# Kernel optimization log

Measured on AMD Instinct MI355X. Metric: run time of the kernel, lower is better.

## Reference

```python
import jax, jax.numpy as jnp
from jax import lax
import numpy as np

ITER_ = 10
SMOOTH = 1.0

# ---------- soft skeletonization (clDice-style, 2D) ----------

def _max_pool(x, wh, ww):
    # x: [B,1,H,W]
    return lax.reduce_window(x, -jnp.inf, lax.max, (1, 1, wh, ww), (1, 1, 1, 1), 'SAME')

def _soft_erode(x):
    return jnp.minimum(-_max_pool(-x, 3, 1), -_max_pool(-x, 1, 3))

def _soft_dilate(x):
    return _max_pool(x, 3, 3)

def _soft_open(x):
    return _soft_dilate(_soft_erode(x))

def soft_skel(img, iters):
    skel = jax.nn.relu(img - _soft_open(img))
    for _ in range(iters):
        img = _soft_erode(img)
        delta = jax.nn.relu(img - _soft_open(img))
        skel = skel + jax.nn.relu(delta - skel * delta)
    return skel

# ---------- exact 2D Euclidean distance transform ----------

def _edt2d(mask):
    # mask: [H,W] bool, True = foreground. distance to nearest background pixel.
    H, W = mask.shape
    BIG = jnp.float32(H + W)
    z = ~mask  # background indicator
    def step(d, zr):
        d = jnp.where(zr, 0.0, jnp.minimum(d + 1.0, BIG))
        return d, d
    init = jnp.full((H,), BIG, jnp.float32)
    _, f = lax.scan(step, init, z.T)            # [W,H] forward along rows
    _, b = lax.scan(step, init, z.T[::-1])      # backward
    g = jnp.minimum(f, b[::-1]).T               # [H,W] 1D row distance
    ys = jnp.arange(H, dtype=jnp.float32)
    diff2 = (ys[:, None] - ys[None, :]) ** 2    # [H,H]
    # lower envelope over columns: d2[y,x] = min_y' g[y',x]^2 + (y-y')^2
    d2 = jnp.min(g[None, :, :] ** 2 + diff2[:, :, None], axis=1)  # [H,W]
    return jnp.sqrt(d2)

_edt_batched = jax.vmap(_edt2d)  # [B,H,W] bool -> [B,H,W] float

# ---------- cbDice pieces ----------

def combine_tensors(A, B, C):
    return jnp.where((A != 0) & (B == 0), A * C, B * C)

def get_weights(mask_input, skel_input, prob_flag):
    # mask_input/skel_input: [B,H,W] float
    mask = mask_input > 0.5
    skel = skel_input > 0.5
    dist = lax.stop_gradient(_edt_batched(mask))       # EDT of binary mask, non-diff
    distances = jnp.where(mask, dist, 0.0)
    skel_radius = jnp.where(skel, distances, 0.0)
    rmax = jnp.maximum(jnp.max(skel_radius, axis=(1, 2), keepdims=True), 1.0)
    rmin = jnp.maximum(jnp.min(skel_radius, axis=(1, 2), keepdims=True), 1.0)
    d_clip = jnp.minimum(distances, rmax)
    dist_map_norm = d_clip / rmax
    skel_R_norm = skel_radius / rmax
    I_norm = (rmax - skel_radius + rmin) / rmax        # dim == 2 branch
    I_norm = jnp.where(skel, I_norm, 0.0)
    if prob_flag:
        return dist_map_norm * mask_input, skel_R_norm * mask_input, I_norm * skel_input
    m = mask.astype(jnp.float32)
    s = skel.astype(jnp.float32)
    return dist_map_norm * m, skel_R_norm * m, I_norm * s

def soft_cb_dice_loss(y_pred, y_true):
    p = jax.nn.sigmoid(y_pred)                              # [B,1,H,W]
    pb = jnp.concatenate([1.0 - p, p], axis=1)              # [B,2,H,W]
    pp = jax.nn.softmax(pb, axis=1)[:, 1]                   # [B,H,W]
    yt = jnp.where(y_true > 0, 1.0, 0.0)[:, 0]              # [B,H,W]
    hard = lax.stop_gradient((pp > 0.5).astype(jnp.float32))
    skel_pred_hard = lax.stop_gradient(soft_skel(hard[:, None], ITER_)[:, 0])
    skel_true = lax.stop_gradient(soft_skel(yt[:, None], ITER_)[:, 0])
    skel_pred_prob = skel_pred_hard * pp
    q_vl, q_slvl, q_sl = get_weights(yt, skel_true, False)
    q_vp, q_spvp, q_sp = get_weights(pp, skel_pred_prob, True)
    w_tprec = (jnp.sum(q_sp * q_vl) + SMOOTH) / (jnp.sum(combine_tensors(q_spvp, q_slvl, q_sp)) + SMOOTH)
    w_tsens = (jnp.sum(q_sl * q_vp) + SMOOTH) / (jnp.sum(combine_tensors(q_slvl, q_spvp, q_sl)) + SMOOTH)
    return 1.0 - 2.0 * (w_tprec * w_tsens) / (w_tprec + w_tsens)

def setup_inputs() -> dict:
    key = jax.random.key(0)
    k1, k2 = jax.random.split(key)
    y_pred = jax.random.normal(k1, (4, 1, 256, 256), dtype=jnp.float32)
    y_true = jax.random.randint(k2, (4, 1, 256, 256), 0, 2, dtype=jnp.int32)
    return {"y_pred": y_pred, "y_true": y_true}

def reference(y_pred, y_true):
    return soft_cb_dice_loss(y_pred, y_true)
```

## Files before the change

### kernel.cpp

```cpp
#include <hip/hip_runtime.h>

typedef unsigned long long u64;

#define NIMG 4
#define H 256
#define W 256
#define NPIX (H*W)
#define NTOT (NIMG*NPIX)
#define WPR 4
#define WPI (H*WPR)
#define WPB (NIMG*WPI)
#define XT 8
#define NSKEL 8
#define NTILE 128
#define NB2 (NSKEL+NTILE)

#define CFLAG(bi)  ((bi)*32)
#define CDONE      256
#define CBAR(img)  (288+(img)*32)
#define RMM(i)     ((i)*32)
#define SUM(i)     ((i)*16)

__device__ __forceinline__ void erode_from(const u64 S[][WPR], int y, u64 out[WPR]) {
  u64 c[WPR], up[WPR], dn[WPR];
#pragma unroll
  for (int k = 0; k < WPR; ++k) {
    c[k]  = S[y][k];
    up[k] = (y > 0)     ? S[y-1][k] : ~0ULL;
    dn[k] = (y < H-1)   ? S[y+1][k] : ~0ULL;
  }
#pragma unroll
  for (int k = 0; k < WPR; ++k) {
    u64 l = (c[k] << 1) | ((k > 0)     ? (c[k-1] >> 63) : 1ULL);
    u64 r = (c[k] >> 1) | ((k < WPR-1) ? (c[k+1] << 63) : 0x8000000000000000ULL);
    out[k] = c[k] & up[k] & dn[k] & l & r;
  }
}

__device__ __forceinline__ void dilate_from(const u64 S[][WPR], int y, u64 out[WPR]) {
  u64 v[WPR];
#pragma unroll
  for (int k = 0; k < WPR; ++k) {
    u64 a = S[y][k];
    if (y > 0)   a |= S[y-1][k];
    if (y < H-1) a |= S[y+1][k];
    v[k] = a;
  }
#pragma unroll
  for (int k = 0; k < WPR; ++k) {
    u64 l = (v[k] << 1) | ((k > 0)     ? (v[k-1] >> 63) : 0ULL);
    u64 r = (v[k] >> 1) | ((k < WPR-1) ? (v[k+1] << 63) : 0ULL);
    out[k] = v[k] | l | r;
  }
}

__global__ void __launch_bounds__(256) prep_kernel(
    const float* __restrict__ y_pred, const int* __restrict__ y_true,
    u64* __restrict__ mask_bits, unsigned* __restrict__ rmm_u,
    double* __restrict__ sums, unsigned* __restrict__ cnts) {
  if (blockIdx.x == 0) {
    if (threadIdx.x < 16) rmm_u[RMM(threadIdx.x)] = (threadIdx.x & 1) ? 0x7F800000u : 0u;
    else if (threadIdx.x < 20) sums[SUM(threadIdx.x - 16)] = 0.0;
    cnts[threadIdx.x] = 0u;
    cnts[256 + threadIdx.x] = 0u;
  }
  int i = blockIdx.x * 256 + threadIdx.x;
  float x = y_pred[i];
  u64 bt = __ballot(y_true[i] > 0);
  u64 bp = __ballot(x > 0.0f);
  if ((threadIdx.x & 63) == 0) {
    mask_bits[i >> 6] = bt;
    mask_bits[WPB + (i >> 6)] = bp;
  }
}

#define EDT_PASS(MROW, DIST, SAVE_MASK)                                        \
  {                                                                            \
    int y = t;                                                                 \
    const u64* row = (MROW) + y*WPR;                                           \
    u64 z[WPR];                                                                \
    _Pragma("unroll")                                                          \
    for (int k = 0; k < WPR; ++k) z[k] = ~row[k];         \
    if (SAVE_MASK) msk_row[y] = row[kx];                                       \
    _Pragma("unroll")                                                          \
    for (int xx = 0; xx < XT; ++xx) {                                          \
      int x = x0 + xx;                                                         \
      int bx = x & 63;                                                         \
      int ld = 512;                                                            \
      {                                                                        \
        u64 w = z[kx] & ((bx == 63) ? ~0ULL : ((1ULL << (bx+1)) - 1ULL));      \
        for (int k = kx; ; ) {                                                 \
          if (w) { int pos = 63 - __builtin_clzll(w) + (k << 6); ld = x - pos; break; } \
          if (--k < 0) break;                                                  \
          w = z[k];                                                            \
        }                                                                      \
      }                                                                        \
      int rd = 512;                                                            \
      {                                                                        \
        u64 w = z[kx] & (~0ULL << bx);                                         \
        for (int k = kx; ; ) {                                                 \
          if (w) { int pos = __builtin_ctzll(w) + (k << 6); rd = pos - x; break; } \
          if (++k > WPR-1) break;                                              \
          w = z[k];                                                            \
        }                                                                      \
      }                                                                        \
      int g = min(ld, rd);                                                     \
      col2[y][xx] = (float)(g * g);                                            \
    }                                                                          \
  }                                                                            \
  __syncthreads();                                                             \
  _Pragma("unroll")                                                            \
  for (int j = 0; j < 8; ++j) {                                                \
    int y = yg * 8 + j;                                                        \
    float best = col2[y][xq];                                                  \
    for (int k = 1; k < H; ++k) {                                              \
      float k2 = (float)(k * k);                                               \
      if (k2 >= best) break;                \
      int ym = y - k, yd = y + k;                                              \
      if (ym >= 0) best = fminf(best, col2[ym][xq] + k2);                      \
      if (yd < H)  best = fminf(best, col2[yd][xq] + k2);                      \
    }                                                                          \
    (DIST)[j] = sqrtf(best);                                                   \
  }                                                                            \
  __syncthreads();

__global__ void __launch_bounds__(256, 1) fused_kernel(
    const float* __restrict__ y_pred, const u64* __restrict__ mask_bits,
    u64* __restrict__ skel_bits, unsigned* __restrict__ rmm_u,
    double* __restrict__ sums, unsigned* __restrict__ cnts,
    float* __restrict__ out) {
  __shared__ u64 SA[H][WPR];
  __shared__ u64 SB[H][WPR];
  __shared__ float col2[H][XT + 1];
  __shared__ u64 srow_t[H];
  __shared__ u64 srow_p[H];
  __shared__ u64 msk_row[H];
  __shared__ float redf[4][4];
  __shared__ unsigned smm[4];
  int t = threadIdx.x;

  if (blockIdx.x < NSKEL) {
    int bi = blockIdx.x;
    int y = t;
    int base = bi * WPI;
    u64 a[WPR], cur[WPR], e[WPR], d[WPR], sk[WPR];
#pragma unroll
    for (int k = 0; k < WPR; ++k) { a[k] = mask_bits[base + y*WPR + k]; SA[y][k] = a[k]; }
    __syncthreads();
    erode_from(SA, y, e);
#pragma unroll
    for (int k = 0; k < WPR; ++k) SB[y][k] = e[k];
    __syncthreads();
    dilate_from(SB, y, d);
#pragma unroll
    for (int k = 0; k < WPR; ++k) { sk[k] = a[k] & ~d[k]; cur[k] = e[k]; }
    u64 (*P)[WPR] = SB;
    u64 (*Q)[WPR] = SA;
    for (int it = 0; it < 10; ++it) {
      erode_from(P, y, e);
#pragma unroll
      for (int k = 0; k < WPR; ++k) Q[y][k] = e[k];
      __syncthreads();
      dilate_from(Q, y, d);
#pragma unroll
      for (int k = 0; k < WPR; ++k) { sk[k] |= cur[k] & ~d[k]; cur[k] = e[k]; }
      u64 (*T)[WPR] = P; P = Q; Q = T;
    }
#pragma unroll
    for (int k = 0; k < WPR; ++k) skel_bits[base + y*WPR + k] = sk[k];
    __syncthreads();
    if (t == 0) {
      __threadfence();
      atomicAdd(&cnts[CFLAG(bi)], 1u);
    }
    return;
  }

  int tb  = blockIdx.x - NSKEL;
  int img = tb >> 5;
  int xt  = tb & 31;
  int x0  = xt * XT;
  int kx  = x0 >> 6;
  int sh0 = x0 & 63;
  int xq  = t & (XT - 1);
  int yg  = t >> 3;

  float dist_t[8], dist_p[8];
  EDT_PASS(mask_bits + img*WPI,       dist_t, 1)
  EDT_PASS(mask_bits + (4+img)*WPI,   dist_p, 0)

  if (t == 0) {
    while (__hip_atomic_load(&cnts[CFLAG(img)], __ATOMIC_RELAXED,
                             __HIP_MEMORY_SCOPE_AGENT) == 0u ||
           __hip_atomic_load(&cnts[CFLAG(4+img)], __ATOMIC_RELAXED,
                             __HIP_MEMORY_SCOPE_AGENT) == 0u)
      __builtin_amdgcn_s_sleep(8);
  }
  __syncthreads();
  srow_t[t] = __hip_atomic_load(&skel_bits[img*WPI + t*WPR + kx],
                                __ATOMIC_RELAXED, __HIP_MEMORY_SCOPE_AGENT);
  srow_p[t] = __hip_atomic_load(&skel_bits[(4+img)*WPI + t*WPR + kx],
                                __ATOMIC_RELAXED, __HIP_MEMORY_SCOPE_AGENT);
  __syncthreads();

  float vmax_t = 0.0f, vmin_t = 3.0e38f, vmax_p = 0.0f, vmin_p = 3.0e38f;
#pragma unroll
  for (int j = 0; j < 8; ++j) {
    int y = yg * 8 + j;
    int sb_t = (int)((srow_t[y] >> (sh0 + xq)) & 1ULL);
    int sb_p = (int)((srow_p[y] >> (sh0 + xq)) & 1ULL);
    float srt = sb_t ? dist_t[j] : 0.0f;
    float srp = sb_p ? dist_p[j] : 0.0f;
    vmax_t = fmaxf(vmax_t, srt); vmin_t = fminf(vmin_t, srt);
    vmax_p = fmaxf(vmax_p, srp); vmin_p = fminf(vmin_p, srp);
  }
  for (int o = 32; o > 0; o >>= 1) {
    vmax_t = fmaxf(vmax_t, __shfl_down(vmax_t, o, 64));
    vmin_t = fminf(vmin_t, __shfl_down(vmin_t, o, 64));
    vmax_p = fmaxf(vmax_p, __shfl_down(vmax_p, o, 64));
    vmin_p = fminf(vmin_p, __shfl_down(vmin_p, o, 64));
  }
  int wave = t >> 6, lane = t & 63;
  if (lane == 0) { redf[wave][0]=vmax_t; redf[wave][1]=vmin_t;
                   redf[wave][2]=vmax_p; redf[wave][3]=vmin_p; }
  __syncthreads();
  if (t == 0) {
    float mxt=redf[0][0], mnt=redf[0][1], mxp=redf[0][2], mnp=redf[0][3];
    for (int wv = 1; wv < 4; ++wv) {
      mxt = fmaxf(mxt, redf[wv][0]); mnt = fminf(mnt, redf[wv][1]);
      mxp = fmaxf(mxp, redf[wv][2]); mnp = fminf(mnp, redf[wv][3]);
    }
    atomicMax(&rmm_u[RMM(img*2 + 0)], __float_as_uint(mxt));
    atomicMin(&rmm_u[RMM(img*2 + 1)], __float_as_uint(mnt));
    atomicMax(&rmm_u[RMM((4+img)*2 + 0)], __float_as_uint(mxp));
    atomicMin(&rmm_u[RMM((4+img)*2 + 1)], __float_as_uint(mnp));
    __hip_atomic_fetch_add(&cnts[CBAR(img)], 1u, __ATOMIC_RELEASE,
                           __HIP_MEMORY_SCOPE_AGENT);
    while (__hip_atomic_load(&cnts[CBAR(img)], __ATOMIC_RELAXED,
                             __HIP_MEMORY_SCOPE_AGENT) < 32u)
      __builtin_amdgcn_s_sleep(8);
  }
  __syncthreads();
  if (t < 4) {
    int idx = (t < 2) ? (img*2 + t) : ((4+img)*2 + (t-2));
    smm[t] = __hip_atomic_load(&rmm_u[RMM(idx)], __ATOMIC_RELAXED,
                               __HIP_MEMORY_SCOPE_AGENT);
  }
  __syncthreads();
  float rmax_t = fmaxf(__uint_as_float(smm[0]), 1.0f);
  float rmin_t = fmaxf(__uint_as_float(smm[1]), 1.0f);
  float rmax_p = fmaxf(__uint_as_float(smm[2]), 1.0f);
  float rmin_p = fmaxf(__uint_as_float(smm[3]), 1.0f);

  float q1 = 0.f, q2 = 0.f, q3 = 0.f, q4 = 0.f;
#pragma unroll
  for (int j = 0; j < 8; ++j) {
    int y = yg * 8 + j;
    float xv = y_pred[img*NPIX + y*W + x0 + xq];
    float p = 1.0f / (1.0f + expf(-xv));
    float ppv = 1.0f / (1.0f + expf(-(2.0f * p - 1.0f)));
    int b = sh0 + xq;
    int m_t  = (int)((msk_row[y] >> b) & 1ULL);
    int s_t  = (int)((srow_t[y] >> b) & 1ULL);
    int s_pb = (int)((srow_p[y] >> b) & 1ULL);
    float distances_t = m_t ? dist_t[j] : 0.0f;
    float skelrad_t   = s_t ? distances_t : 0.0f;
    float dmn_t = fminf(distances_t, rmax_t) / rmax_t;
    float srn_t = skelrad_t / rmax_t;
    float In_t  = s_t ? (rmax_t - skelrad_t + rmin_t) / rmax_t : 0.0f;
    float q_vl   = m_t ? dmn_t : 0.0f;
    float q_slvl = m_t ? srn_t : 0.0f;
    float q_sl   = s_t ? In_t  : 0.0f;
    float skel_in_p = s_pb ? ppv : 0.0f;
    bool msk_p = ppv > 0.5f;
    bool sk_p  = skel_in_p > 0.5f;
    float distances_p = msk_p ? dist_p[j] : 0.0f;
    float skelrad_p   = sk_p ? distances_p : 0.0f;
    float dmn_p = fminf(distances_p, rmax_p) / rmax_p;
    float srn_p = skelrad_p / rmax_p;
    float In_p  = sk_p ? (rmax_p - skelrad_p + rmin_p) / rmax_p : 0.0f;
    float q_vp   = dmn_p * ppv;
    float q_spvp = srn_p * ppv;
    float q_sp   = In_p * skel_in_p;
    q1 += q_sp * q_vl;
    q2 += (q_spvp != 0.0f && q_slvl == 0.0f) ? q_spvp * q_sp : q_slvl * q_sp;
    q3 += q_sl * q_vp;
    q4 += (q_slvl != 0.0f && q_spvp == 0.0f) ? q_slvl * q_sl : q_spvp * q_sl;
  }
  for (int o = 32; o > 0; o >>= 1) {
    q1 += __shfl_down(q1, o, 64);
    q2 += __shfl_down(q2, o, 64);
    q3 += __shfl_down(q3, o, 64);
    q4 += __shfl_down(q4, o, 64);
  }
  if (lane == 0) { redf[wave][0]=q1; redf[wave][1]=q2; redf[wave][2]=q3; redf[wave][3]=q4; }
  __syncthreads();
  if (t == 0) {
    float a0=0,a1=0,a2=0,a3=0;
    for (int wv = 0; wv < 4; ++wv) {
      a0 += redf[wv][0]; a1 += redf[wv][1]; a2 += redf[wv][2]; a3 += redf[wv][3];
    }
    atomicAdd(&sums[SUM(0)], (double)a0);
    atomicAdd(&sums[SUM(1)], (double)a1);
    atomicAdd(&sums[SUM(2)], (double)a2);
    atomicAdd(&sums[SUM(3)], (double)a3);
    __threadfence();
    unsigned c = atomicAdd(&cnts[CDONE], 1u);
    if (c == NTILE - 1) {
      double s0 = atomicAdd(&sums[SUM(0)], 0.0);
      double s1 = atomicAdd(&sums[SUM(1)], 0.0);
      double s2 = atomicAdd(&sums[SUM(2)], 0.0);
      double s3 = atomicAdd(&sums[SUM(3)], 0.0);
      double wp  = (s0 + 1.0) / (s1 + 1.0);
      double wsn = (s2 + 1.0) / (s3 + 1.0);
      out[0] = (float)(1.0 - 2.0 * (wp * wsn) / (wp + wsn));
    }
  }
}

extern "C" void kernel_launch(void* const* d_in, const int* in_sizes, int n_in,
                              void* d_out, int out_size, void* d_ws, size_t ws_size,
                              hipStream_t stream) {
  (void)in_sizes; (void)n_in; (void)out_size; (void)ws_size;
  const float* y_pred = (const float*)d_in[0];
  const int*   y_true = (const int*)d_in[1];
  float* out = (float*)d_out;
  char* ws = (char*)d_ws;

  u64*   mask_bits = (u64*)  (ws + 0);
  u64*   skel_bits = (u64*)  (ws + 65536);
  unsigned* rmm_u  = (unsigned*)(ws + 131072);
  double* sums     = (double*)(ws + 133120);
  unsigned* cnts   = (unsigned*)(ws + 133632);

  prep_kernel<<<NTOT/256, 256, 0, stream>>>(y_pred, y_true, mask_bits, rmm_u, sums, cnts);
  fused_kernel<<<NB2, 256, 0, stream>>>(y_pred, mask_bits, skel_bits, rmm_u, sums, cnts, out);
}
```

Baseline: 80.47 us.

## Fuse mask bit-packing into main kernel with per-image grid barrier

Removes the separate prep kernel. The EDT tile blocks now pack the y_true and y_pred threshold bits themselves and publish them through relaxed atomic stores. A per-image counter barrier makes both the EDT and skeleton blocks wait until all 32 tiles of their image have written their masks. Counter and min/max initialisation moves to a hipMemsetAsync, and atomicMin is replaced by atomicMax on inverted bits so zero-init works. This saves one kernel launch and a global round trip, but adds a spin barrier that relies on all blocks being co-resident and delays the skeleton blocks until the mask is ready.

Measured after the change: 82.84 us. 3.0% more time.

```diff
diff --git a/kernel.cpp b/kernel.cpp
--- a/kernel.cpp
+++ b/kernel.cpp
@@ -18,6 +18,7 @@
 #define CFLAG(bi)  ((bi)*32)
 #define CDONE      256
 #define CBAR(img)  (288+(img)*32)
+#define CMASK(img) (416+(img)*32)
 #define RMM(i)     ((i)*32)
 #define SUM(i)     ((i)*16)
 
@@ -54,34 +55,18 @@
   }
 }
 
-__global__ void __launch_bounds__(256) prep_kernel(
-    const float* __restrict__ y_pred, const int* __restrict__ y_true,
-    u64* __restrict__ mask_bits, unsigned* __restrict__ rmm_u,
-    double* __restrict__ sums, unsigned* __restrict__ cnts) {
-  if (blockIdx.x == 0) {
-    if (threadIdx.x < 16) rmm_u[RMM(threadIdx.x)] = (threadIdx.x & 1) ? 0x7F800000u : 0u;
-    else if (threadIdx.x < 20) sums[SUM(threadIdx.x - 16)] = 0.0;
-    cnts[threadIdx.x] = 0u;
-    cnts[256 + threadIdx.x] = 0u;
-  }
-  int i = blockIdx.x * 256 + threadIdx.x;
-  float x = y_pred[i];
-  u64 bt = __ballot(y_true[i] > 0);
-  u64 bp = __ballot(x > 0.0f);
-  if ((threadIdx.x & 63) == 0) {
-    mask_bits[i >> 6] = bt;
-    mask_bits[WPB + (i >> 6)] = bp;
-  }
-}
-
-#define EDT_PASS(MROW, DIST, SAVE_MASK)                                        \
+#define EDT_PASS(WBASE, DIST, SAVE_MASK)                                       \
   {                                                                            \
     int y = t;                                                                 \
-    const u64* row = (MROW) + y*WPR;                                           \
+    const u64* row = mask_bits + (WBASE) + y*WPR;                              \
     u64 z[WPR];                                                                \
     _Pragma("unroll")                                                          \
-    for (int k = 0; k < WPR; ++k) z[k] = ~row[k];         \
-    if (SAVE_MASK) msk_row[y] = row[kx];                                       \
+    for (int k = 0; k < WPR; ++k) {                                            \
+      u64 m = __hip_atomic_load(&row[k], __ATOMIC_RELAXED,                     \
+                                __HIP_MEMORY_SCOPE_AGENT);                     \
+      if (SAVE_MASK && k == kx) msk_row[y] = m;                                \
+      z[k] = ~m;                                          \
+    }                                                                          \
     _Pragma("unroll")                                                          \
     for (int xx = 0; xx < XT; ++xx) {                                          \
       int x = x0 + xx;                                                         \
@@ -125,10 +110,10 @@
   __syncthreads();
 
 __global__ void __launch_bounds__(256, 1) fused_kernel(
-    const float* __restrict__ y_pred, const u64* __restrict__ mask_bits,
-    u64* __restrict__ skel_bits, unsigned* __restrict__ rmm_u,
-    double* __restrict__ sums, unsigned* __restrict__ cnts,
-    float* __restrict__ out) {
+    const float* __restrict__ y_pred, const int* __restrict__ y_true,
+    u64* __restrict__ mask_bits, u64* __restrict__ skel_bits,
+    unsigned* __restrict__ rmm_u, double* __restrict__ sums,
+    unsigned* __restrict__ cnts, float* __restrict__ out) {
   __shared__ u64 SA[H][WPR];
   __shared__ u64 SB[H][WPR];
   __shared__ float col2[H][XT + 1];
@@ -137,15 +122,27 @@
   __shared__ u64 msk_row[H];
   __shared__ float redf[4][4];
   __shared__ unsigned smm[4];
+  __shared__ unsigned char mbuf[2][256];
   int t = threadIdx.x;
 
   if (blockIdx.x < NSKEL) {
-    int bi = blockIdx.x;
+    int bi  = blockIdx.x;
+    int img = bi & 3;
+    if (t == 0) {
+      while (__hip_atomic_load(&cnts[CMASK(img)], __ATOMIC_RELAXED,
+                               __HIP_MEMORY_SCOPE_AGENT) < 32u)
+        __builtin_amdgcn_s_sleep(8);
+    }
+    __syncthreads();
     int y = t;
     int base = bi * WPI;
     u64 a[WPR], cur[WPR], e[WPR], d[WPR], sk[WPR];
 #pragma unroll
-    for (int k = 0; k < WPR; ++k) { a[k] = mask_bits[base + y*WPR + k]; SA[y][k] = a[k]; }
+    for (int k = 0; k < WPR; ++k) {
+      a[k] = __hip_atomic_load(&mask_bits[base + y*WPR + k],
+                               __ATOMIC_RELAXED, __HIP_MEMORY_SCOPE_AGENT);
+      SA[y][k] = a[k];
+    }
     __syncthreads();
     erode_from(SA, y, e);
 #pragma unroll
@@ -185,9 +182,44 @@
   int xq  = t & (XT - 1);
   int yg  = t >> 3;
 
+  {
+    int px0 = img * NPIX + xt * 2048;
+    const int4*   ti = (const int4*)(y_true + px0 + t * 8);
+    const float4* pf = (const float4*)(y_pred + px0 + t * 8);
+    int4   a0 = ti[0], a1 = ti[1];
+    float4 f0 = pf[0], f1 = pf[1];
+    unsigned bt = (unsigned)(a0.x > 0)        | ((unsigned)(a0.y > 0) << 1)
+                | ((unsigned)(a0.z > 0) << 2) | ((unsigned)(a0.w > 0) << 3)
+                | ((unsigned)(a1.x > 0) << 4) | ((unsigned)(a1.y > 0) << 5)
+                | ((unsigned)(a1.z > 0) << 6) | ((unsigned)(a1.w > 0) << 7);
+    unsigned bp = (unsigned)(f0.x > 0.0f)        | ((unsigned)(f0.y > 0.0f) << 1)
+                | ((unsigned)(f0.z > 0.0f) << 2) | ((unsigned)(f0.w > 0.0f) << 3)
+                | ((unsigned)(f1.x > 0.0f) << 4) | ((unsigned)(f1.y > 0.0f) << 5)
+                | ((unsigned)(f1.z > 0.0f) << 6) | ((unsigned)(f1.w > 0.0f) << 7);
+    mbuf[0][t] = (unsigned char)bt;
+    mbuf[1][t] = (unsigned char)bp;
+  }
+  __syncthreads();
+  if (t < 64) {
+    u64 w = ((const u64*)mbuf)[t];
+    int wbase = img * WPI + xt * 32;
+    u64* dst = (t < 32) ? &mask_bits[wbase + t]
+                        : &mask_bits[WPB + wbase + (t - 32)];
+    __hip_atomic_store(dst, w, __ATOMIC_RELAXED, __HIP_MEMORY_SCOPE_AGENT);
+  }
+  __syncthreads();
+  if (t == 0) {
+    __hip_atomic_fetch_add(&cnts[CMASK(img)], 1u, __ATOMIC_RELEASE,
+                           __HIP_MEMORY_SCOPE_AGENT);
+    while (__hip_atomic_load(&cnts[CMASK(img)], __ATOMIC_RELAXED,
+                             __HIP_MEMORY_SCOPE_AGENT) < 32u)
+      __builtin_amdgcn_s_sleep(8);
+  }
+  __syncthreads();
+
   float dist_t[8], dist_p[8];
-  EDT_PASS(mask_bits + img*WPI,       dist_t, 1)
-  EDT_PASS(mask_bits + (4+img)*WPI,   dist_p, 0)
+  EDT_PASS(img*WPI,     dist_t, 1)
+  EDT_PASS((4+img)*WPI, dist_p, 0)
 
   if (t == 0) {
     while (__hip_atomic_load(&cnts[CFLAG(img)], __ATOMIC_RELAXED,
@@ -230,10 +262,10 @@
       mxt = fmaxf(mxt, redf[wv][0]); mnt = fminf(mnt, redf[wv][1]);
       mxp = fmaxf(mxp, redf[wv][2]); mnp = fminf(mnp, redf[wv][3]);
     }
-    atomicMax(&rmm_u[RMM(img*2 + 0)], __float_as_uint(mxt));
-    atomicMin(&rmm_u[RMM(img*2 + 1)], __float_as_uint(mnt));
+    atomicMax(&rmm_u[RMM(img*2 + 0)],     __float_as_uint(mxt));
+    atomicMax(&rmm_u[RMM(img*2 + 1)],     ~__float_as_uint(mnt));
     atomicMax(&rmm_u[RMM((4+img)*2 + 0)], __float_as_uint(mxp));
-    atomicMin(&rmm_u[RMM((4+img)*2 + 1)], __float_as_uint(mnp));
+    atomicMax(&rmm_u[RMM((4+img)*2 + 1)], ~__float_as_uint(mnp));
     __hip_atomic_fetch_add(&cnts[CBAR(img)], 1u, __ATOMIC_RELEASE,
                            __HIP_MEMORY_SCOPE_AGENT);
     while (__hip_atomic_load(&cnts[CBAR(img)], __ATOMIC_RELAXED,
@@ -247,10 +279,10 @@
                                __HIP_MEMORY_SCOPE_AGENT);
   }
   __syncthreads();
-  float rmax_t = fmaxf(__uint_as_float(smm[0]), 1.0f);
-  float rmin_t = fmaxf(__uint_as_float(smm[1]), 1.0f);
-  float rmax_p = fmaxf(__uint_as_float(smm[2]), 1.0f);
-  float rmin_p = fmaxf(__uint_as_float(smm[3]), 1.0f);
+  float rmax_t = fmaxf(__uint_as_float( smm[0]), 1.0f);
+  float rmin_t = fmaxf(__uint_as_float(~smm[1]), 1.0f);
+  float rmax_p = fmaxf(__uint_as_float( smm[2]), 1.0f);
+  float rmin_p = fmaxf(__uint_as_float(~smm[3]), 1.0f);
 
   float q1 = 0.f, q2 = 0.f, q3 = 0.f, q4 = 0.f;
 #pragma unroll
@@ -333,6 +365,7 @@
   double* sums     = (double*)(ws + 133120);
   unsigned* cnts   = (unsigned*)(ws + 133632);
 
-  prep_kernel<<<NTOT/256, 256, 0, stream>>>(y_pred, y_true, mask_bits, rmm_u, sums, cnts);
-  fused_kernel<<<NB2, 256, 0, stream>>>(y_pred, mask_bits, skel_bits, rmm_u, sums, cnts, out);
+  hipMemsetAsync(ws + 131072, 0, 5120, stream);
+  fused_kernel<<<NB2, 256, 0, stream>>>(y_pred, y_true, mask_bits, skel_bits,
+                                        rmm_u, sums, cnts, out);
 }
```
